# Kernel optimization log

Hardware: AMD Instinct MI355X
Metric: run time of the kernel (lower is better)

The kernel has to match this reference:

```python
import jax, jax.numpy as jnp
import numpy as np

DIM = 512
NUM_HEADS = 8
HEAD_DIM = DIM // NUM_HEADS
EPS = 1e-12  # F.normalize eps


def _l2norm(x):
    # F.normalize(x, dim=-1): x / max(||x||, eps)
    n = jnp.sqrt(jnp.sum(x * x, axis=-1, keepdims=True))
    return x / jnp.maximum(n, EPS)


def setup_inputs() -> dict:
    key = jax.random.key(0)
    ks = jax.random.split(key, 5)
    B, T, D = 4, 2048, DIM
    z = jax.random.normal(ks[0], (B, T, D), dtype=jnp.float32)
    t = jnp.zeros((1,), dtype=jnp.float32)  # unused ODE time
    omega = jax.random.normal(ks[1], (1, 1, D), dtype=jnp.float32) * 0.1
    # nn.Linear default init scale ~ U(-1/sqrt(fan_in), 1/sqrt(fan_in))
    s = 1.0 / np.sqrt(D)
    W_qk = jax.random.uniform(ks[2], (2 * D, D), jnp.float32, -s, s)
    W_out = jax.random.uniform(ks[3], (D, D), jnp.float32, -s, s)
    b_out = jax.random.uniform(ks[4], (D,), jnp.float32, -s, s)
    return {"t": t, "z": z, "omega": omega, "W_qk": W_qk, "W_out": W_out, "b_out": b_out}


def reference(t, z, omega, W_qk, W_out, b_out):
    B, T, D = z.shape
    H, hd = NUM_HEADS, HEAD_DIM
    qk = z @ W_qk.T                      # [B,T,2D]
    q, k = qk[..., :D], qk[..., D:]
    q = _l2norm(q.reshape(B, T, H, hd))  # [B,T,H,hd]
    k = _l2norm(k.reshape(B, T, H, hd))
    # coupling: [B,H,T,T]
    coupling = jnp.einsum("bqhd,bkhd->bhqk", q, k)
    interaction = jnp.sin(coupling)
    force = jnp.einsum("bhqk,bkhd->bqhd", interaction, k).reshape(B, T, D)
    return omega + force @ W_out.T + b_out
```

## Files before the change

kernel.cpp:

```cpp
#include <hip/hip_runtime.h>
#include <hip/hip_bf16.h>

typedef unsigned short u16;
typedef __attribute__((ext_vector_type(8))) short short8;
typedef __attribute__((ext_vector_type(4))) short short4_;
typedef __attribute__((ext_vector_type(4))) float f32x4;

#define B_ 4
#define T_ 2048
#define D_ 512
#define H_ 8
#define M_ (B_*T_)
#define INV2PI 0.15915494309189535f

__device__ u16   g_qb[M_*D_];
__device__ u16   g_kb[M_*D_];
__device__ u16   g_kTp[(size_t)B_*H_*64*T_];
__device__ float g_fA[(size_t)M_*D_];
__device__ float g_fB[(size_t)M_*D_];

__device__ inline u16 f2bf(float f) {
  union { __hip_bfloat16 h; u16 u; } cv;
  cv.h = __float2bfloat16(f);
  return cv.u;
}

__device__ inline float sin2pi(float x) {
#if __has_builtin(__builtin_amdgcn_sinf)
  return __builtin_amdgcn_sinf(x);
#else
  return __sinf(x * 6.283185307179586f);
#endif
}

__device__ inline short8 cvt8(f32x4 a, f32x4 b) {
  short8 o;
  o[0]=(short)f2bf(a[0]); o[1]=(short)f2bf(a[1]); o[2]=(short)f2bf(a[2]); o[3]=(short)f2bf(a[3]);
  o[4]=(short)f2bf(b[0]); o[5]=(short)f2bf(b[1]); o[6]=(short)f2bf(b[2]); o[7]=(short)f2bf(b[3]);
  return o;
}

__device__ inline int perm5(int p) {
  int lg = p >> 3, e = p & 7;
  return (e < 4) ? lg*4 + e : 16 + lg*4 + (e & 3);
}

template<int MODE>
__global__ __launch_bounds__(256, 2)
void gemm_bt(float* __restrict__ Cout, const float* __restrict__ add1,
             const float* __restrict__ add2, const float* __restrict__ Afp,
             const float* __restrict__ Bfp) {
  constexpr int K = 512;
  constexpr int N = (MODE == 0) ? 1024 : 512;
  __shared__ u16 As[128*72];
  __shared__ u16 Bs[128*72];
  const int m0 = blockIdx.x*128, n0 = blockIdx.y*128;
  const int t = threadIdx.x;
  const int w = t>>6, l = t&63;
  const int wr = (w>>1)*64, wc = (w&1)*64;
  const int lg = l>>4, li = l&15;
  const int srow = t>>3, scol = (t&7)*8;

  f32x4 acc[4][4] = {};

  for (int k0 = 0; k0 < K; k0 += 64) {
#pragma unroll
    for (int p = 0; p < 4; ++p) {
      int r = srow + p*32;
      {
        f32x4 b0 = *(const f32x4*)&Bfp[(size_t)(n0+r)*K + k0 + scol];
        f32x4 b1 = *(const f32x4*)&Bfp[(size_t)(n0+r)*K + k0 + scol + 4];
        *(short8*)&Bs[r*72 + scol] = cvt8(b0, b1);
      }
      if (MODE == 0) {
        f32x4 a0 = *(const f32x4*)&Afp[(size_t)(m0+r)*K + k0 + scol];
        f32x4 a1 = *(const f32x4*)&Afp[(size_t)(m0+r)*K + k0 + scol + 4];
        *(short8*)&As[r*72 + scol] = cvt8(a0, a1);
      } else {
        size_t off = (size_t)(m0+r)*K + k0 + scol;
        f32x4 a0 = *(const f32x4*)&g_fA[off];
        f32x4 a1 = *(const f32x4*)&g_fA[off+4];
        f32x4 c0 = *(const f32x4*)&g_fB[off];
        f32x4 c1 = *(const f32x4*)&g_fB[off+4];
        a0 += c0; a1 += c1;
        *(short8*)&As[r*72 + scol] = cvt8(a0, a1);
      }
    }
    __syncthreads();
#pragma unroll
    for (int ks = 0; ks < 2; ++ks) {
      short8 af[4], bf[4];
#pragma unroll
      for (int i = 0; i < 4; ++i)
        af[i] = *(const short8*)&As[(wr + i*16 + li)*72 + ks*32 + lg*8];
#pragma unroll
      for (int j = 0; j < 4; ++j)
        bf[j] = *(const short8*)&Bs[(wc + j*16 + li)*72 + ks*32 + lg*8];
#pragma unroll
      for (int i = 0; i < 4; ++i)
#pragma unroll
        for (int j = 0; j < 4; ++j)
          acc[i][j] = __builtin_amdgcn_mfma_f32_16x16x32_bf16(af[i], bf[j], acc[i][j], 0, 0, 0);
    }
    __syncthreads();
  }

  if (MODE == 0) {
    const bool isq = (n0 < 512);
    u16* dst = isq ? g_qb : g_kb;
    const float qs = isq ? INV2PI : 1.0f;
    const int nb = (isq ? n0 : n0 - 512) + wc;
#pragma unroll
    for (int i = 0; i < 4; ++i) {
#pragma unroll
      for (int r = 0; r < 4; ++r) {
        float s = 0.f;
#pragma unroll
        for (int j = 0; j < 4; ++j) s += acc[i][j][r]*acc[i][j][r];
#pragma unroll
        for (int off = 1; off < 16; off <<= 1) s += __shfl_xor(s, off);
        float sc = qs / fmaxf(sqrtf(s), 1e-12f);
        int row = m0 + wr + i*16 + lg*4 + r;
#pragma unroll
        for (int j = 0; j < 4; ++j)
          dst[(size_t)row*D_ + nb + j*16 + li] = f2bf(acc[i][j][r]*sc);
      }
    }
  } else {
#pragma unroll
    for (int i = 0; i < 4; ++i) {
#pragma unroll
      for (int j = 0; j < 4; ++j) {
        int col = n0 + wc + j*16 + li;
        float badd = add1[col] + add2[col];
#pragma unroll
        for (int r = 0; r < 4; ++r) {
          int row = m0 + wr + i*16 + lg*4 + r;
          Cout[(size_t)row*N + col] = acc[i][j][r] + badd;
        }
      }
    }
  }
}

__global__ void transpose_k_kernel() {
  __shared__ u16 tile[64*72];
  const int t0 = blockIdx.x*64, bh = blockIdx.y;
  const int b = bh>>3, h = bh&7;
  const int t = threadIdx.x;
  {
    int r = t>>2, cs = (t&3)*16;
    const u16* src = g_kb + (size_t)(b*T_ + t0 + r)*D_ + h*64 + cs;
    *(short8*)&tile[r*72 + cs]     = *(const short8*)(src);
    *(short8*)&tile[r*72 + cs + 8] = *(const short8*)(src + 8);
  }
  __syncthreads();
  {
    int d = t>>2, ts = (t&3)*16;
    short8 o0, o1;
#pragma unroll
    for (int j = 0; j < 8; ++j) {
      int p0 = ts + j, p1 = ts + 8 + j;
      int s0 = (p0 & ~31) | perm5(p0 & 31);
      int s1 = (p1 & ~31) | perm5(p1 & 31);
      o0[j] = (short)tile[s0*72 + d];
      o1[j] = (short)tile[s1*72 + d];
    }
    u16* dst = g_kTp + ((size_t)bh*64 + d)*T_ + t0 + ts;
    *(short8*)(dst)     = o0;
    *(short8*)(dst + 8) = o1;
  }
}

__global__ __launch_bounds__(256, 4)
void kuramoto_attn_kernel() {
  __shared__ u16 Ks[128*72];
  __shared__ u16 KTs[64*136];
  const int wg  = blockIdx.x;
  const int wgp = (wg & 7)*128 + (wg >> 3);
  const int bh = wgp >> 5, qt = (wgp & 31) >> 1, kh = wgp & 1;
  const int b = bh >> 3, h = bh & 7;
  const int t = threadIdx.x;
  const int w = t>>6, l = t&63;
  const int lg = l>>4, li = l&15;

  short8 bq[2][2];
#pragma unroll
  for (int ks = 0; ks < 2; ++ks)
#pragma unroll
    for (int j = 0; j < 2; ++j)
      bq[ks][j] = *(const short8*)&g_qb[(size_t)(b*T_ + qt*128 + w*32 + j*16 + li)*D_
                                        + h*64 + ks*32 + lg*8];

  f32x4 acc_o[2][4] = {};

  for (int kt = kh*8; kt < kh*8 + 8; ++kt) {
    __syncthreads();
    {
      int r = t>>3, cs = (t&7)*8;
#pragma unroll
      for (int p = 0; p < 4; ++p) {
        int rr = r + p*32;
        *(short8*)&Ks[rr*72 + cs] =
          *(const short8*)&g_kb[(size_t)(b*T_ + kt*128 + rr)*D_ + h*64 + cs];
      }
      int d = t>>4, ks2 = (t&15)*8;
#pragma unroll
      for (int p = 0; p < 4; ++p) {
        int dd = d + p*16;
        *(short8*)&KTs[dd*136 + ks2] =
          *(const short8*)&g_kTp[((size_t)bh*64 + dd)*T_ + kt*128 + ks2];
      }
    }
    __syncthreads();

#pragma unroll
    for (int kkp = 0; kkp < 4; ++kkp) {
      f32x4 sacc[2][2] = {};
#pragma unroll
      for (int ks = 0; ks < 2; ++ks) {
        short8 af0 = *(const short8*)&Ks[((2*kkp  )*16 + li)*72 + ks*32 + lg*8];
        short8 af1 = *(const short8*)&Ks[((2*kkp+1)*16 + li)*72 + ks*32 + lg*8];
#pragma unroll
        for (int j = 0; j < 2; ++j) {
          sacc[0][j] = __builtin_amdgcn_mfma_f32_16x16x32_bf16(af0, bq[ks][j], sacc[0][j], 0,0,0);
          sacc[1][j] = __builtin_amdgcn_mfma_f32_16x16x32_bf16(af1, bq[ks][j], sacc[1][j], 0,0,0);
        }
      }
      short8 apv[2];
#pragma unroll
      for (int j = 0; j < 2; ++j) {
        union { unsigned int u[4]; short8 s; } cv;
        cv.u[0] = (unsigned)f2bf(sin2pi(sacc[0][j][0])) | ((unsigned)f2bf(sin2pi(sacc[0][j][1]))<<16);
        cv.u[1] = (unsigned)f2bf(sin2pi(sacc[0][j][2])) | ((unsigned)f2bf(sin2pi(sacc[0][j][3]))<<16);
        cv.u[2] = (unsigned)f2bf(sin2pi(sacc[1][j][0])) | ((unsigned)f2bf(sin2pi(sacc[1][j][1]))<<16);
        cv.u[3] = (unsigned)f2bf(sin2pi(sacc[1][j][2])) | ((unsigned)f2bf(sin2pi(sacc[1][j][3]))<<16);
        apv[j] = cv.s;
      }
#pragma unroll
      for (int di = 0; di < 4; ++di) {
        short8 bv = *(const short8*)&KTs[(di*16 + li)*136 + kkp*32 + lg*8];
#pragma unroll
        for (int j = 0; j < 2; ++j)
          acc_o[j][di] = __builtin_amdgcn_mfma_f32_16x16x32_bf16(apv[j], bv, acc_o[j][di], 0,0,0);
      }
    }
  }

  float* F = kh ? g_fB : g_fA;
#pragma unroll
  for (int j = 0; j < 2; ++j)
#pragma unroll
    for (int di = 0; di < 4; ++di)
#pragma unroll
      for (int r = 0; r < 4; ++r) {
        int row = b*T_ + qt*128 + w*32 + j*16 + lg*4 + r;
        int col = h*64 + di*16 + li;
        F[(size_t)row*D_ + col] = acc_o[j][di][r];
      }
}

extern "C" void kernel_launch(void* const* d_in, const int* in_sizes, int n_in,
                              void* d_out, int out_size, void* d_ws, size_t ws_size,
                              hipStream_t stream) {
  const float* z     = (const float*)d_in[1];
  const float* omega = (const float*)d_in[2];
  const float* Wqk   = (const float*)d_in[3];
  const float* Wout  = (const float*)d_in[4];
  const float* bout  = (const float*)d_in[5];
  float* out = (float*)d_out;

  gemm_bt<0><<<dim3(M_/128, 1024/128), 256, 0, stream>>>(nullptr, nullptr, nullptr, z, Wqk);
  transpose_k_kernel<<<dim3(T_/64, B_*H_), 256, 0, stream>>>();
  kuramoto_attn_kernel<<<1024, 256, 0, stream>>>();
  gemm_bt<1><<<dim3(M_/128, 512/128), 256, 0, stream>>>(out, omega, bout, nullptr, Wout);
}
```

Before: 168.8 us.

## Double-buffer K tiles and double query rows per workgroup in attention kernel

The attention kernel now handles 256 query rows per workgroup, with each wave owning 64 rows instead of 32, which halves the grid to 512 blocks. Each staged K/K^T tile is therefore reused across twice as many queries. K and K^T tiles are double-buffered in LDS: the next tile is loaded into registers before the MFMA work on the current one and written to the other buffer afterwards, leaving one barrier per iteration instead of two. The cost is more registers and LDS per block (occupancy hint drops from 4 to 2) and fewer workgroups to spread across the GPU's compute units.

```diff
diff --git a/kernel.cpp b/kernel.cpp
--- a/kernel.cpp
+++ b/kernel.cpp
@@ -172,64 +172,72 @@
   }
 }
 
-__global__ __launch_bounds__(256, 4)
+__global__ __launch_bounds__(256, 2)
 void kuramoto_attn_kernel() {
-  __shared__ u16 Ks[128*72];
-  __shared__ u16 KTs[64*136];
+  __shared__ u16 Ks[2][128*72];
+  __shared__ u16 KTs[2][64*136];
   const int wg  = blockIdx.x;
-  const int wgp = (wg & 7)*128 + (wg >> 3);
-  const int bh = wgp >> 5, qt = (wgp & 31) >> 1, kh = wgp & 1;
+  const int wgp = (wg & 7)*64 + (wg >> 3);
+  const int bh = wgp >> 4, qt = (wgp & 15) >> 1, kh = wgp & 1;
   const int b = bh >> 3, h = bh & 7;
   const int t = threadIdx.x;
   const int w = t>>6, l = t&63;
   const int lg = l>>4, li = l&15;
 
-  short8 bq[2][2];
+  short8 bq[2][4];
 #pragma unroll
   for (int ks = 0; ks < 2; ++ks)
 #pragma unroll
-    for (int j = 0; j < 2; ++j)
-      bq[ks][j] = *(const short8*)&g_qb[(size_t)(b*T_ + qt*128 + w*32 + j*16 + li)*D_
+    for (int j = 0; j < 4; ++j)
+      bq[ks][j] = *(const short8*)&g_qb[(size_t)(b*T_ + qt*256 + w*64 + j*16 + li)*D_
                                         + h*64 + ks*32 + lg*8];
 
-  f32x4 acc_o[2][4] = {};
-
-  for (int kt = kh*8; kt < kh*8 + 8; ++kt) {
-    __syncthreads();
-    {
-      int r = t>>3, cs = (t&7)*8;
+  const int sr = t>>3, sc = (t&7)*8;
+  const int sd = t>>4, sk = (t&15)*8;
+  const u16* kbase = g_kb  + (size_t)b*T_*D_ + h*64;
+  const u16* tbase = g_kTp + (size_t)bh*64*T_;
+  const int kt0 = kh*8;
+
+  f32x4 acc_o[4][4] = {};
+
+#pragma unroll
+  for (int p = 0; p < 4; ++p) {
+    *(short8*)&Ks[0][(sr + p*32)*72 + sc] =
+      *(const short8*)&kbase[(size_t)(kt0*128 + sr + p*32)*D_ + sc];
+    *(short8*)&KTs[0][(sd + p*16)*136 + sk] =
+      *(const short8*)&tbase[(size_t)(sd + p*16)*T_ + kt0*128 + sk];
+  }
+  __syncthreads();
+
+#pragma unroll 2
+  for (int ii = 0; ii < 8; ++ii) {
+    const int buf = ii & 1;
+    short8 rk[4], rt[4];
+    if (ii < 7) {
+      const int ktn = kt0 + ii + 1;
 #pragma unroll
       for (int p = 0; p < 4; ++p) {
-        int rr = r + p*32;
-        *(short8*)&Ks[rr*72 + cs] =
-          *(const short8*)&g_kb[(size_t)(b*T_ + kt*128 + rr)*D_ + h*64 + cs];
-      }
-      int d = t>>4, ks2 = (t&15)*8;
-#pragma unroll
-      for (int p = 0; p < 4; ++p) {
-        int dd = d + p*16;
-        *(short8*)&KTs[dd*136 + ks2] =
-          *(const short8*)&g_kTp[((size_t)bh*64 + dd)*T_ + kt*128 + ks2];
-      }
-    }
-    __syncthreads();
+        rk[p] = *(const short8*)&kbase[(size_t)(ktn*128 + sr + p*32)*D_ + sc];
+        rt[p] = *(const short8*)&tbase[(size_t)(sd + p*16)*T_ + ktn*128 + sk];
+      }
+    }
 
 #pragma unroll
     for (int kkp = 0; kkp < 4; ++kkp) {
-      f32x4 sacc[2][2] = {};
+      f32x4 sacc[2][4] = {};
 #pragma unroll
       for (int ks = 0; ks < 2; ++ks) {
-        short8 af0 = *(const short8*)&Ks[((2*kkp  )*16 + li)*72 + ks*32 + lg*8];
-        short8 af1 = *(const short8*)&Ks[((2*kkp+1)*16 + li)*72 + ks*32 + lg*8];
-#pragma unroll
-        for (int j = 0; j < 2; ++j) {
+        short8 af0 = *(const short8*)&Ks[buf][((2*kkp  )*16 + li)*72 + ks*32 + lg*8];
+        short8 af1 = *(const short8*)&Ks[buf][((2*kkp+1)*16 + li)*72 + ks*32 + lg*8];
+#pragma unroll
+        for (int j = 0; j < 4; ++j) {
           sacc[0][j] = __builtin_amdgcn_mfma_f32_16x16x32_bf16(af0, bq[ks][j], sacc[0][j], 0,0,0);
           sacc[1][j] = __builtin_amdgcn_mfma_f32_16x16x32_bf16(af1, bq[ks][j], sacc[1][j], 0,0,0);
         }
       }
-      short8 apv[2];
-#pragma unroll
-      for (int j = 0; j < 2; ++j) {
+      short8 apv[4];
+#pragma unroll
+      for (int j = 0; j < 4; ++j) {
         union { unsigned int u[4]; short8 s; } cv;
         cv.u[0] = (unsigned)f2bf(sin2pi(sacc[0][j][0])) | ((unsigned)f2bf(sin2pi(sacc[0][j][1]))<<16);
         cv.u[1] = (unsigned)f2bf(sin2pi(sacc[0][j][2])) | ((unsigned)f2bf(sin2pi(sacc[0][j][3]))<<16);
@@ -239,22 +247,31 @@
       }
 #pragma unroll
       for (int di = 0; di < 4; ++di) {
-        short8 bv = *(const short8*)&KTs[(di*16 + li)*136 + kkp*32 + lg*8];
-#pragma unroll
-        for (int j = 0; j < 2; ++j)
+        short8 bv = *(const short8*)&KTs[buf][(di*16 + li)*136 + kkp*32 + lg*8];
+#pragma unroll
+        for (int j = 0; j < 4; ++j)
           acc_o[j][di] = __builtin_amdgcn_mfma_f32_16x16x32_bf16(apv[j], bv, acc_o[j][di], 0,0,0);
       }
     }
+
+    if (ii < 7) {
+#pragma unroll
+      for (int p = 0; p < 4; ++p) {
+        *(short8*)&Ks[buf^1][(sr + p*32)*72 + sc] = rk[p];
+        *(short8*)&KTs[buf^1][(sd + p*16)*136 + sk] = rt[p];
+      }
+    }
+    __syncthreads();
   }
 
   float* F = kh ? g_fB : g_fA;
 #pragma unroll
-  for (int j = 0; j < 2; ++j)
+  for (int j = 0; j < 4; ++j)
 #pragma unroll
     for (int di = 0; di < 4; ++di)
 #pragma unroll
       for (int r = 0; r < 4; ++r) {
-        int row = b*T_ + qt*128 + w*32 + j*16 + lg*4 + r;
+        int row = b*T_ + qt*256 + w*64 + j*16 + lg*4 + r;
         int col = h*64 + di*16 + li;
         F[(size_t)row*D_ + col] = acc_o[j][di][r];
       }
@@ -272,6 +289,6 @@
 
   gemm_bt<0><<<dim3(M_/128, 1024/128), 256, 0, stream>>>(nullptr, nullptr, nullptr, z, Wqk);
   transpose_k_kernel<<<dim3(T_/64, B_*H_), 256, 0, stream>>>();
-  kuramoto_attn_kernel<<<1024, 256, 0, stream>>>();
+  kuramoto_attn_kernel<<<512, 256, 0, stream>>>();
   gemm_bt<1><<<dim3(M_/128, 512/128), 256, 0, stream>>>(out, omega, bout, nullptr, Wout);
 }
```

New measurement: 160.1 us. -5.2%, faster.
